# Performance work log

Hardware: AMD Instinct MI355X
Metric: run time of the kernel (lower is better)

Reference implementation:

```python
import jax, jax.numpy as jnp
import numpy as np

N_NODES = 50000
N_EDGES = 640000
HIDDEN = 128
LN_EPS = 1e-5


def setup_inputs() -> dict:
    key = jax.random.key(0)
    k_h, k_e, k_w1, k_w2 = jax.random.split(key, 4)
    s = 1.0 / np.sqrt(HIDDEN)
    return {
        "h": jax.random.normal(k_h, (N_NODES, HIDDEN), dtype=jnp.float32),
        "edge_index": jax.random.randint(k_e, (2, N_EDGES), 0, N_NODES, dtype=jnp.int32),
        "W1": jax.random.normal(k_w1, (HIDDEN, HIDDEN), dtype=jnp.float32) * s,
        "b1": jnp.zeros((HIDDEN,), dtype=jnp.float32),
        "W2": jax.random.normal(k_w2, (HIDDEN, HIDDEN), dtype=jnp.float32) * s,
        "b2": jnp.zeros((HIDDEN,), dtype=jnp.float32),
        "eps": jnp.zeros((), dtype=jnp.float32),  # GINConv train_eps init
        "gamma": jnp.ones((HIDDEN,), dtype=jnp.float32),
        "beta": jnp.zeros((HIDDEN,), dtype=jnp.float32),
    }


def reference(h, edge_index, W1, b1, W2, b2, eps, gamma, beta):
    src, dst = edge_index[0], edge_index[1]
    # GIN aggregation: sum of neighbor features scattered to destination nodes
    agg = jax.ops.segment_sum(h[src], dst, num_segments=h.shape[0])  # (N, D)
    z = (1.0 + eps) * h + agg
    # 2-layer MLP: Linear -> ReLU -> Linear (torch Linear: x @ W.T + b)
    z = jax.nn.relu(z @ W1.T + b1)
    h_conv = z @ W2.T + b2
    # residual + LayerNorm + ReLU (dropout is identity in eval mode)
    h_res = h_conv + h
    mu = jnp.mean(h_res, axis=-1, keepdims=True)
    var = jnp.var(h_res, axis=-1, keepdims=True)
    h_norm = (h_res - mu) * jax.lax.rsqrt(var + LN_EPS) * gamma + beta
    return jax.nn.relu(h_norm)
```

## Files before the change

kernel.cpp:

```cpp
#include <hip/hip_runtime.h>

#define HID 128
#define LN_EPS 1e-5f
#define LDSW 136

typedef __attribute__((ext_vector_type(8))) short bf16x8;
typedef __attribute__((ext_vector_type(4))) float f32x4;

static __device__ __forceinline__ unsigned short f2bf(float f) {
  unsigned int x = __float_as_uint(f);
  x += 0x7fffu + ((x >> 16) & 1u);
  return (unsigned short)(x >> 16);
}
static __device__ __forceinline__ float bflo(unsigned int u) { return __uint_as_float(u << 16); }
static __device__ __forceinline__ float bfhi(unsigned int u) { return __uint_as_float(u & 0xffff0000u); }

__global__ __launch_bounds__(256) void k_count(const int* __restrict__ ei,
                                               int* __restrict__ counts, int nE) {
  const int e = blockIdx.x * 256 + threadIdx.x;
  if (e >= nE) return;
  atomicAdd(&counts[ei[nE + e]], 1);
}

__global__ __launch_bounds__(256) void k_scan1(const int* __restrict__ counts,
                                               int* __restrict__ offsets,
                                               int* __restrict__ bsum, int n) {
  __shared__ int sm[256];
  const int t = threadIdx.x;
  const int i = blockIdx.x * 256 + t;
  const int v = (i < n) ? counts[i] : 0;
  int incl = v;
  sm[t] = incl;
  __syncthreads();
#pragma unroll
  for (int off = 1; off < 256; off <<= 1) {
    const int other = (t >= off) ? sm[t - off] : 0;
    __syncthreads();
    incl += other;
    sm[t] = incl;
    __syncthreads();
  }
  if (i < n) offsets[i] = incl - v;
  if (t == 255) bsum[blockIdx.x] = incl;
}

__global__ __launch_bounds__(256) void k_scan2(const int* __restrict__ bsum,
                                               int* __restrict__ ebase,
                                               int* __restrict__ offsets,
                                               int nb, int n) {
  __shared__ int sm[256];
  const int t = threadIdx.x;
  const int v = (t < nb) ? bsum[t] : 0;
  int incl = v;
  sm[t] = incl;
  __syncthreads();
#pragma unroll
  for (int off = 1; off < 256; off <<= 1) {
    const int other = (t >= off) ? sm[t - off] : 0;
    __syncthreads();
    incl += other;
    sm[t] = incl;
    __syncthreads();
  }
  if (t < nb) ebase[t] = incl - v;
  if (t == 255) offsets[n] = incl;
}

__global__ __launch_bounds__(256) void k_scan3(int* __restrict__ offsets,
                                               int* __restrict__ cursors,
                                               const int* __restrict__ ebase, int n) {
  const int i = blockIdx.x * 256 + threadIdx.x;
  if (i >= n) return;
  const int o = offsets[i] + ebase[blockIdx.x];
  offsets[i] = o;
  cursors[i] = o;
}

__global__ __launch_bounds__(256) void k_bucket(const int* __restrict__ ei,
                                                int* __restrict__ cursors,
                                                int* __restrict__ esrc, int nE) {
  const int e = blockIdx.x * 256 + threadIdx.x;
  if (e >= nE) return;
  const int s = ei[e];
  const int d = ei[nE + e];
  const int pos = atomicAdd(&cursors[d], 1);
  esrc[pos] = s;
}

__global__ __launch_bounds__(256) void k_tobf3(const float* __restrict__ h,
                                               const float* __restrict__ w1,
                                               const float* __restrict__ w2,
                                               uint2* __restrict__ hb,
                                               uint2* __restrict__ w1b,
                                               uint2* __restrict__ w2b,
                                               int nh4, int nw4) {
  const int total = nh4 + 2 * nw4;
  const int stride = gridDim.x * 256;
  for (int i = blockIdx.x * 256 + threadIdx.x; i < total; i += stride) {
    const float* src;
    uint2* dst;
    int off;
    if (i < nh4) { src = h; dst = hb; off = i; }
    else if (i < nh4 + nw4) { src = w1; dst = w1b; off = i - nh4; }
    else { src = w2; dst = w2b; off = i - nh4 - nw4; }
    const float4 v = reinterpret_cast<const float4*>(src)[off];
    uint2 p;
    p.x = (unsigned)f2bf(v.x) | ((unsigned)f2bf(v.y) << 16);
    p.y = (unsigned)f2bf(v.z) | ((unsigned)f2bf(v.w) << 16);
    dst[off] = p;
  }
}

__global__ __launch_bounds__(256) void k_gather(const unsigned short* __restrict__ hbf,
                                                const int* __restrict__ offsets,
                                                const int* __restrict__ esrc,
                                                const float* __restrict__ eps,
                                                unsigned short* __restrict__ zbf, int nNodes) {
  const int gid = blockIdx.x * 256 + threadIdx.x;
  const int node = gid >> 5;
  if (node >= nNodes) return;
  const int col4 = (threadIdx.x & 31) * 4;
  const float c = 1.0f + eps[0];

  const uint2 hv = *reinterpret_cast<const uint2*>(hbf + (size_t)node * HID + col4);
  float a0 = c * bflo(hv.x), a1 = c * bfhi(hv.x);
  float a2 = c * bflo(hv.y), a3 = c * bfhi(hv.y);

  const int beg = offsets[node], end = offsets[node + 1];
  int e = beg;
  for (; e + 1 < end; e += 2) {
    const int s0 = esrc[e], s1 = esrc[e + 1];
    const uint2 v0 = *reinterpret_cast<const uint2*>(hbf + (size_t)s0 * HID + col4);
    const uint2 v1 = *reinterpret_cast<const uint2*>(hbf + (size_t)s1 * HID + col4);
    a0 += bflo(v0.x) + bflo(v1.x);
    a1 += bfhi(v0.x) + bfhi(v1.x);
    a2 += bflo(v0.y) + bflo(v1.y);
    a3 += bfhi(v0.y) + bfhi(v1.y);
  }
  if (e < end) {
    const uint2 v0 = *reinterpret_cast<const uint2*>(hbf + (size_t)esrc[e] * HID + col4);
    a0 += bflo(v0.x); a1 += bfhi(v0.x); a2 += bflo(v0.y); a3 += bfhi(v0.y);
  }
  uint2 o;
  o.x = (unsigned)f2bf(a0) | ((unsigned)f2bf(a1) << 16);
  o.y = (unsigned)f2bf(a2) | ((unsigned)f2bf(a3) << 16);
  *reinterpret_cast<uint2*>(zbf + (size_t)node * HID + col4) = o;
}

__global__ __launch_bounds__(256) void k_mmf(const unsigned short* __restrict__ zbf,
                                             const unsigned short* __restrict__ w1,
                                             const unsigned short* __restrict__ w2,
                                             const float* __restrict__ b1,
                                             const float* __restrict__ b2,
                                             const float* __restrict__ h,
                                             const float* __restrict__ gamma,
                                             const float* __restrict__ beta,
                                             float* __restrict__ out, int nTiles) {
  __shared__ unsigned short yt[16][LDSW];
  __shared__ float lnp[16][4][2];
  const int wave = threadIdx.x >> 6;
  const int l = threadIdx.x & 63;
  const int mtile = blockIdx.x;
  if (mtile >= nTiles) return;
  const int row0 = mtile * 16;
  const int lr = l & 15;
  const int lq = l >> 4;

  bf16x8 a[4];
#pragma unroll
  for (int ks = 0; ks < 4; ++ks)
    a[ks] = *reinterpret_cast<const bf16x8*>(zbf + (size_t)(row0 + lr) * HID + ks * 32 + lq * 8);

  f32x4 acc[2];
#pragma unroll
  for (int j = 0; j < 2; ++j) acc[j] = (f32x4){0.f, 0.f, 0.f, 0.f};
#pragma unroll
  for (int j = 0; j < 2; ++j) {
    const int nt = wave * 2 + j;
    const unsigned short* wb = w1 + (size_t)(nt * 16 + lr) * HID + lq * 8;
#pragma unroll
    for (int ks = 0; ks < 4; ++ks) {
      const bf16x8 b = *reinterpret_cast<const bf16x8*>(wb + ks * 32);
      acc[j] = __builtin_amdgcn_mfma_f32_16x16x32_bf16(a[ks], b, acc[j], 0, 0, 0);
    }
  }

#pragma unroll
  for (int j = 0; j < 2; ++j) {
    const int cc = (wave * 2 + j) * 16 + lr;
    const float bs = b1[cc];
#pragma unroll
    for (int r = 0; r < 4; ++r)
      yt[lq * 4 + r][cc] = f2bf(fmaxf(acc[j][r] + bs, 0.f));
  }
  __syncthreads();

  bf16x8 a2[4];
#pragma unroll
  for (int ks = 0; ks < 4; ++ks)
    a2[ks] = *reinterpret_cast<const bf16x8*>(&yt[lr][ks * 32 + lq * 8]);

#pragma unroll
  for (int j = 0; j < 2; ++j) acc[j] = (f32x4){0.f, 0.f, 0.f, 0.f};
#pragma unroll
  for (int j = 0; j < 2; ++j) {
    const int nt = wave * 2 + j;
    const unsigned short* wb = w2 + (size_t)(nt * 16 + lr) * HID + lq * 8;
#pragma unroll
    for (int ks = 0; ks < 4; ++ks) {
      const bf16x8 b = *reinterpret_cast<const bf16x8*>(wb + ks * 32);
      acc[j] = __builtin_amdgcn_mfma_f32_16x16x32_bf16(a2[ks], b, acc[j], 0, 0, 0);
    }
  }

#pragma unroll
  for (int j = 0; j < 2; ++j) {
    const int cc = (wave * 2 + j) * 16 + lr;
    const float bs = b2[cc];
#pragma unroll
    for (int r = 0; r < 4; ++r) {
      const int row = row0 + lq * 4 + r;
      acc[j][r] += bs + h[(size_t)row * HID + cc];
    }
  }

#pragma unroll
  for (int r = 0; r < 4; ++r) {
    float s = acc[0][r] + acc[1][r];
    float ss = acc[0][r] * acc[0][r] + acc[1][r] * acc[1][r];
#pragma unroll
    for (int m = 1; m < 16; m <<= 1) {
      s += __shfl_xor(s, m, 64);
      ss += __shfl_xor(ss, m, 64);
    }
    if (lr == 0) {
      lnp[lq * 4 + r][wave][0] = s;
      lnp[lq * 4 + r][wave][1] = ss;
    }
  }
  __syncthreads();

  float mu_[4], rstd_[4];
#pragma unroll
  for (int r = 0; r < 4; ++r) {
    const int rt = lq * 4 + r;
    float s = 0.f, ss = 0.f;
#pragma unroll
    for (int w = 0; w < 4; ++w) {
      const float2 p = *reinterpret_cast<const float2*>(&lnp[rt][w][0]);
      s += p.x;
      ss += p.y;
    }
    const float mu = s * (1.f / 128.f);
    const float var = ss * (1.f / 128.f) - mu * mu;
    mu_[r] = mu;
    rstd_[r] = rsqrtf(var + LN_EPS);
  }
#pragma unroll
  for (int j = 0; j < 2; ++j) {
    const int cc = (wave * 2 + j) * 16 + lr;
    const float g = gamma[cc], be = beta[cc];
#pragma unroll
    for (int r = 0; r < 4; ++r) {
      const int row = row0 + lq * 4 + r;
      const float o = (acc[j][r] - mu_[r]) * rstd_[r] * g + be;
      out[(size_t)row * HID + cc] = fmaxf(o, 0.f);
    }
  }
}

extern "C" void kernel_launch(void* const* d_in, const int* in_sizes, int n_in,
                              void* d_out, int out_size, void* d_ws, size_t ws_size,
                              hipStream_t stream) {
  const float* h     = (const float*)d_in[0];
  const int*   ei    = (const int*)d_in[1];
  const float* W1    = (const float*)d_in[2];
  const float* b1    = (const float*)d_in[3];
  const float* W2    = (const float*)d_in[4];
  const float* b2    = (const float*)d_in[5];
  const float* eps   = (const float*)d_in[6];
  const float* gamma = (const float*)d_in[7];
  const float* beta  = (const float*)d_in[8];

  const int nNodes = in_sizes[0] / HID;
  const int nE     = in_sizes[1] / 2;
  const int nb     = (nNodes + 255) / 256;

  int* counts  = (int*)d_ws;
  int* offsets = counts + nNodes;
  int* cursors = offsets + nNodes + 1;
  int* bsum    = cursors + nNodes;
  int* ebase   = bsum + nb;
  int* esrc    = counts + 150400;
  unsigned short* hbf  = (unsigned short*)(esrc + nE);
  unsigned short* zbf  = hbf + (size_t)nNodes * HID;
  unsigned short* w1bf = zbf + (size_t)nNodes * HID;
  unsigned short* w2bf = w1bf + HID * HID;

  hipMemsetAsync(counts, 0, (size_t)nNodes * sizeof(int), stream);

  const int eblocks = (nE + 255) / 256;
  k_tobf3<<<2048, 256, 0, stream>>>(h, W1, W2, (uint2*)hbf, (uint2*)w1bf, (uint2*)w2bf,
                                    nNodes * HID / 4, HID * HID / 4);
  k_count<<<eblocks, 256, 0, stream>>>(ei, counts, nE);
  k_scan1<<<nb, 256, 0, stream>>>(counts, offsets, bsum, nNodes);
  k_scan2<<<1, 256, 0, stream>>>(bsum, ebase, offsets, nb, nNodes);
  k_scan3<<<nb, 256, 0, stream>>>(offsets, cursors, ebase, nNodes);
  k_bucket<<<eblocks, 256, 0, stream>>>(ei, cursors, esrc, nE);

  k_gather<<<(nNodes * 32 + 255) / 256, 256, 0, stream>>>(hbf, offsets, esrc, eps, zbf, nNodes);

  const int nTiles = nNodes / 16;
  k_mmf<<<nTiles, 256, 0, stream>>>(zbf, w1bf, w2bf, b1, b2, h, gamma, beta,
                                    (float*)d_out, nTiles);
}
```

Before: 243.2 us.

## Fuse bf16 conversion with edge counting and replace bucket atomics with rank scatter

The edge-degree counting is merged into the bf16 conversion kernel as extra blocks, and each edge's atomicAdd return value is saved as its rank within its destination bucket. The bucketing pass then writes edges straight to offsets[d]+rank[e] with no second round of atomics, and the cursors array is dropped. This saves one kernel launch and one set of contended atomics, at the cost of writing and reading an extra per-edge rank array.

New measurement: 212.7 us. 12.5% less time.

```diff
diff --git a/kernel.cpp b/kernel.cpp
--- a/kernel.cpp
+++ b/kernel.cpp
@@ -15,88 +15,28 @@
 static __device__ __forceinline__ float bflo(unsigned int u) { return __uint_as_float(u << 16); }
 static __device__ __forceinline__ float bfhi(unsigned int u) { return __uint_as_float(u & 0xffff0000u); }
 
-__global__ __launch_bounds__(256) void k_count(const int* __restrict__ ei,
-                                               int* __restrict__ counts, int nE) {
-  const int e = blockIdx.x * 256 + threadIdx.x;
-  if (e >= nE) return;
-  atomicAdd(&counts[ei[nE + e]], 1);
-}
-
-__global__ __launch_bounds__(256) void k_scan1(const int* __restrict__ counts,
-                                               int* __restrict__ offsets,
-                                               int* __restrict__ bsum, int n) {
-  __shared__ int sm[256];
-  const int t = threadIdx.x;
-  const int i = blockIdx.x * 256 + t;
-  const int v = (i < n) ? counts[i] : 0;
-  int incl = v;
-  sm[t] = incl;
-  __syncthreads();
-#pragma unroll
-  for (int off = 1; off < 256; off <<= 1) {
-    const int other = (t >= off) ? sm[t - off] : 0;
-    __syncthreads();
-    incl += other;
-    sm[t] = incl;
-    __syncthreads();
-  }
-  if (i < n) offsets[i] = incl - v;
-  if (t == 255) bsum[blockIdx.x] = incl;
-}
-
-__global__ __launch_bounds__(256) void k_scan2(const int* __restrict__ bsum,
-                                               int* __restrict__ ebase,
-                                               int* __restrict__ offsets,
-                                               int nb, int n) {
-  __shared__ int sm[256];
-  const int t = threadIdx.x;
-  const int v = (t < nb) ? bsum[t] : 0;
-  int incl = v;
-  sm[t] = incl;
-  __syncthreads();
-#pragma unroll
-  for (int off = 1; off < 256; off <<= 1) {
-    const int other = (t >= off) ? sm[t - off] : 0;
-    __syncthreads();
-    incl += other;
-    sm[t] = incl;
-    __syncthreads();
-  }
-  if (t < nb) ebase[t] = incl - v;
-  if (t == 255) offsets[n] = incl;
-}
-
-__global__ __launch_bounds__(256) void k_scan3(int* __restrict__ offsets,
-                                               int* __restrict__ cursors,
-                                               const int* __restrict__ ebase, int n) {
-  const int i = blockIdx.x * 256 + threadIdx.x;
-  if (i >= n) return;
-  const int o = offsets[i] + ebase[blockIdx.x];
-  offsets[i] = o;
-  cursors[i] = o;
-}
-
-__global__ __launch_bounds__(256) void k_bucket(const int* __restrict__ ei,
-                                                int* __restrict__ cursors,
-                                                int* __restrict__ esrc, int nE) {
-  const int e = blockIdx.x * 256 + threadIdx.x;
-  if (e >= nE) return;
-  const int s = ei[e];
-  const int d = ei[nE + e];
-  const int pos = atomicAdd(&cursors[d], 1);
-  esrc[pos] = s;
-}
-
-__global__ __launch_bounds__(256) void k_tobf3(const float* __restrict__ h,
-                                               const float* __restrict__ w1,
-                                               const float* __restrict__ w2,
-                                               uint2* __restrict__ hb,
-                                               uint2* __restrict__ w1b,
-                                               uint2* __restrict__ w2b,
-                                               int nh4, int nw4) {
+__global__ __launch_bounds__(256) void k_cvt_rank(const float* __restrict__ h,
+                                                  const float* __restrict__ w1,
+                                                  const float* __restrict__ w2,
+                                                  uint2* __restrict__ hb,
+                                                  uint2* __restrict__ w1b,
+                                                  uint2* __restrict__ w2b,
+                                                  int nh4, int nw4,
+                                                  const int* __restrict__ ei,
+                                                  int* __restrict__ counts,
+                                                  int* __restrict__ rank,
+                                                  int nE, int EB) {
+  if ((int)blockIdx.x < EB) {
+    const int e = blockIdx.x * 256 + threadIdx.x;
+    if (e < nE) {
+      const int d = ei[nE + e];
+      rank[e] = atomicAdd(&counts[d], 1);
+    }
+    return;
+  }
   const int total = nh4 + 2 * nw4;
-  const int stride = gridDim.x * 256;
-  for (int i = blockIdx.x * 256 + threadIdx.x; i < total; i += stride) {
+  const int stride = (gridDim.x - EB) * 256;
+  for (int i = (blockIdx.x - EB) * 256 + threadIdx.x; i < total; i += stride) {
     const float* src;
     uint2* dst;
     int off;
@@ -109,6 +49,67 @@
     p.y = (unsigned)f2bf(v.z) | ((unsigned)f2bf(v.w) << 16);
     dst[off] = p;
   }
+}
+
+__global__ __launch_bounds__(256) void k_scan1(const int* __restrict__ counts,
+                                               int* __restrict__ offsets,
+                                               int* __restrict__ bsum, int n) {
+  __shared__ int sm[256];
+  const int t = threadIdx.x;
+  const int i = blockIdx.x * 256 + t;
+  const int v = (i < n) ? counts[i] : 0;
+  int incl = v;
+  sm[t] = incl;
+  __syncthreads();
+#pragma unroll
+  for (int off = 1; off < 256; off <<= 1) {
+    const int other = (t >= off) ? sm[t - off] : 0;
+    __syncthreads();
+    incl += other;
+    sm[t] = incl;
+    __syncthreads();
+  }
+  if (i < n) offsets[i] = incl - v;
+  if (t == 255) bsum[blockIdx.x] = incl;
+}
+
+__global__ __launch_bounds__(256) void k_scan2(const int* __restrict__ bsum,
+                                               int* __restrict__ ebase,
+                                               int* __restrict__ offsets,
+                                               int nb, int n) {
+  __shared__ int sm[256];
+  const int t = threadIdx.x;
+  const int v = (t < nb) ? bsum[t] : 0;
+  int incl = v;
+  sm[t] = incl;
+  __syncthreads();
+#pragma unroll
+  for (int off = 1; off < 256; off <<= 1) {
+    const int other = (t >= off) ? sm[t - off] : 0;
+    __syncthreads();
+    incl += other;
+    sm[t] = incl;
+    __syncthreads();
+  }
+  if (t < nb) ebase[t] = incl - v;
+  if (t == 255) offsets[n] = incl;
+}
+
+__global__ __launch_bounds__(256) void k_scan3(int* __restrict__ offsets,
+                                               const int* __restrict__ ebase, int n) {
+  const int i = blockIdx.x * 256 + threadIdx.x;
+  if (i >= n) return;
+  offsets[i] += ebase[blockIdx.x];
+}
+
+__global__ __launch_bounds__(256) void k_scat(const int* __restrict__ ei,
+                                              const int* __restrict__ rank,
+                                              const int* __restrict__ offsets,
+                                              int* __restrict__ esrc, int nE) {
+  const int e = blockIdx.x * 256 + threadIdx.x;
+  if (e >= nE) return;
+  const int d = ei[nE + e];
+  esrc[offsets[d] + rank[e]] = ei[e];
 }
 
 __global__ __launch_bounds__(256) void k_gather(const unsigned short* __restrict__ hbf,
@@ -285,13 +286,15 @@
   const int nNodes = in_sizes[0] / HID;
   const int nE     = in_sizes[1] / 2;
   const int nb     = (nNodes + 255) / 256;
+  const int nh4    = nNodes * HID / 4;
+  const int nw4    = HID * HID / 4;
 
   int* counts  = (int*)d_ws;
   int* offsets = counts + nNodes;
-  int* cursors = offsets + nNodes + 1;
-  int* bsum    = cursors + nNodes;
+  int* bsum    = offsets + nNodes + 1;
   int* ebase   = bsum + nb;
-  int* esrc    = counts + 150400;
+  int* rank    = counts + 100800;
+  int* esrc    = rank + nE;
   unsigned short* hbf  = (unsigned short*)(esrc + nE);
   unsigned short* zbf  = hbf + (size_t)nNodes * HID;
   unsigned short* w1bf = zbf + (size_t)nNodes * HID;
@@ -299,14 +302,13 @@
 
   hipMemsetAsync(counts, 0, (size_t)nNodes * sizeof(int), stream);
 
-  const int eblocks = (nE + 255) / 256;
-  k_tobf3<<<2048, 256, 0, stream>>>(h, W1, W2, (uint2*)hbf, (uint2*)w1bf, (uint2*)w2bf,
-                                    nNodes * HID / 4, HID * HID / 4);
-  k_count<<<eblocks, 256, 0, stream>>>(ei, counts, nE);
+  const int EB = (nE + 255) / 256;
+  k_cvt_rank<<<EB + 2048, 256, 0, stream>>>(h, W1, W2, (uint2*)hbf, (uint2*)w1bf, (uint2*)w2bf,
+                                            nh4, nw4, ei, counts, rank, nE, EB);
   k_scan1<<<nb, 256, 0, stream>>>(counts, offsets, bsum, nNodes);
   k_scan2<<<1, 256, 0, stream>>>(bsum, ebase, offsets, nb, nNodes);
-  k_scan3<<<nb, 256, 0, stream>>>(offsets, cursors, ebase, nNodes);
-  k_bucket<<<eblocks, 256, 0, stream>>>(ei, cursors, esrc, nE);
+  k_scan3<<<nb, 256, 0, stream>>>(offsets, ebase, nNodes);
+  k_scat<<<EB, 256, 0, stream>>>(ei, rank, offsets, esrc, nE);
 
   k_gather<<<(nNodes * 32 + 255) / 256, 256, 0, stream>>>(hbf, offsets, esrc, eps, zbf, nNodes);
 
```
